# Optimization experiments

Measured on AMD Instinct MI355X. Metric: run time of the kernel, lower is better.

The kernel has to match this reference:

```python
import jax, jax.numpy as jnp
import numpy as np

BN_EPS = 1e-5


def setup_inputs() -> dict:
    key = jax.random.key(0)
    ks = jax.random.split(key, 12)
    B, N, d_e, d_a = 16, 2048, 256, 64
    s_e = 1.0 / np.sqrt(d_e)
    return {
        "x":    jax.random.normal(ks[0], (B, N, d_e), dtype=jnp.float32),
        "Wq":   jax.random.uniform(ks[1], (d_e, d_a), jnp.float32, -s_e, s_e),
        "bq":   jax.random.uniform(ks[2], (d_a,), jnp.float32, -s_e, s_e),
        "Wk":   jax.random.uniform(ks[3], (d_e, d_a), jnp.float32, -s_e, s_e),
        "bk":   jax.random.uniform(ks[4], (d_a,), jnp.float32, -s_e, s_e),
        "Wv":   jax.random.uniform(ks[5], (d_e, d_e), jnp.float32, -s_e, s_e),
        "bv":   jax.random.uniform(ks[6], (d_e,), jnp.float32, -s_e, s_e),
        "Wl":   jax.random.uniform(ks[7], (d_e, d_e), jnp.float32, -s_e, s_e),
        "bl":   jax.random.uniform(ks[8], (d_e,), jnp.float32, -s_e, s_e),
        "gamma": jnp.ones((d_e,), jnp.float32),
        "beta":  jnp.zeros((d_e,), jnp.float32),
    }


def reference(x, Wq, bq, Wk, bk, Wv, bv, Wl, bl, gamma, beta):
    # x: [B, N, d_e]
    q = x @ Wq + bq          # [B, N, d_a]
    k = x @ Wk + bk          # [B, N, d_a]
    v = x @ Wv + bv          # [B, N, d_e]
    d_a = q.shape[-1]
    # NOTE: PCT scales by d_a, not sqrt(d_a) -- faithful to the source.
    score = jnp.einsum('bnd,bmd->bnm', q, k) / jnp.asarray(d_a, q.dtype)
    score = jax.nn.softmax(score, axis=2)          # [B, N, N]
    attn = jnp.einsum('bnm,bmd->bnd', score, v)    # [B, N, d_e]
    # LBR: linear + BatchNorm1d (training-mode batch stats over B,N) + ReLU
    h = attn @ Wl + bl                             # [B, N, d_e]
    mean = jnp.mean(h, axis=(0, 1))
    var = jnp.mean((h - mean) ** 2, axis=(0, 1))   # biased variance (torch BN)
    y = jax.nn.relu((h - mean) * jax.lax.rsqrt(var + BN_EPS) * gamma + beta)
    return y + x
```

## Files before the change

### kernel.cpp

```cpp
#include <hip/hip_runtime.h>
#include <hip/hip_bf16.h>

#define B_  16
#define N_  2048
#define DE  256
#define DA  64
#define T_  (B_*N_)

typedef __attribute__((ext_vector_type(4)))  float f32x4;
typedef __attribute__((ext_vector_type(8)))  short bf16x8;
typedef unsigned short u16;
typedef unsigned long long u64;

__device__ __forceinline__ float bf2f(u16 x){
  unsigned v = ((unsigned)x) << 16;
  return __builtin_bit_cast(float, v);
}
__device__ __forceinline__ u16 f2bf(float f){
  unsigned u = __builtin_bit_cast(unsigned, f);
  u += 0x7fffu + ((u >> 16) & 1u);
  return (u16)(u >> 16);
}
__device__ __forceinline__ unsigned cvtpk(float a, float b){
  unsigned r;
  asm("v_cvt_pk_bf16_f32 %0, %1, %2" : "=v"(r) : "v"(a), "v"(b));
  return r;
}
__device__ __forceinline__ f32x4 mfma16(bf16x8 a, bf16x8 b, f32x4 c){
  return __builtin_amdgcn_mfma_f32_16x16x32_bf16(a, b, c, 0, 0, 0);
}
__device__ __forceinline__ bool is_f32(const void* gsig){
  return *(const unsigned*)gsig == 0x3F800000u;
}
__device__ __forceinline__ float gload(const void* p, long i, bool f32m){
  return f32m ? ((const float*)p)[i] : bf2f(((const u16*)p)[i]);
}

__global__ void k_prep(const void* __restrict__ Wq, const void* __restrict__ Wk,
                       const void* __restrict__ Wv, const void* __restrict__ Wl,
                       const void* __restrict__ bq, const void* __restrict__ bk,
                       const void* __restrict__ bv, const void* __restrict__ bl,
                       const void* __restrict__ gsig,
                       u16* __restrict__ Wt, u16* __restrict__ Wlt,
                       float* __restrict__ bqkv, float* __restrict__ blf){
  bool f32m = is_f32(gsig);
  int i = blockIdx.x*256 + threadIdx.x;
  if (i < 384*256){
    int n = i/256, kk = i%256;
    float v;
    if (n < 64)       v = gload(Wq, (long)kk*64 + n, f32m);
    else if (n < 128) v = gload(Wk, (long)kk*64 + (n-64), f32m);
    else              v = gload(Wv, (long)kk*256 + (n-128), f32m);
    Wt[i] = f2bf(v);
  }
  int j = i - 384*256;
  if (j >= 0 && j < 256*256){
    int n = j/256, kk = j%256;
    Wlt[j] = f2bf(gload(Wl, (long)kk*256 + n, f32m));
  }
  int m = i - (384*256 + 256*256);
  if (m >= 0 && m < 384){
    float v;
    if (m < 64)       v = gload(bq, m, f32m);
    else if (m < 128) v = gload(bk, m-64, f32m);
    else              v = gload(bv, m-128, f32m);
    bqkv[m] = v;
  }
  int p = i - (384*256 + 256*256 + 384);
  if (p >= 0 && p < 256) blf[p] = gload(bl, p, f32m);
}

__global__ __launch_bounds__(256) void k_qkv(
    const void* __restrict__ xg, const void* __restrict__ gsig,
    const u16* __restrict__ Wt, const float* __restrict__ bqkv,
    u16* __restrict__ qo, u16* __restrict__ ko, u16* __restrict__ vtt){
  __shared__ __align__(16) u16 sm[256*72];
  bool f32m = is_f32(gsig);
  int tid = threadIdx.x, lane = tid & 63, w = tid >> 6;
  int lm = lane & 15, lq = lane >> 4;
  long t0 = (long)blockIdx.x * 64;

  #pragma unroll
  for(int it=0; it<8; it++){
    int c = tid + 256*it;
    int tok = c >> 5, kk = (c & 31)*8;
    bf16x8 d;
    if (f32m){
      const float* xf = (const float*)xg + (t0+tok)*DE + kk;
      f32x4 a = *(const f32x4*)xf;
      f32x4 b2 = *(const f32x4*)(xf+4);
      #pragma unroll
      for(int j2=0;j2<4;j2++){ d[j2]=(short)f2bf(a[j2]); d[4+j2]=(short)f2bf(b2[j2]); }
    } else {
      d = *(const bf16x8*)((const u16*)xg + (t0+tok)*DE + kk);
    }
    *(bf16x8*)(sm + tok*264 + kk) = d;
  }
  __syncthreads();

  f32x4 acc[4][6];
  #pragma unroll
  for(int mt=0;mt<4;mt++)
    #pragma unroll
    for(int nt=0;nt<6;nt++){ acc[mt][nt][0]=0.f;acc[mt][nt][1]=0.f;acc[mt][nt][2]=0.f;acc[mt][nt][3]=0.f; }

  for(int s=0;s<8;s++){
    int kk = s*32 + lq*8;
    bf16x8 afr[4];
    #pragma unroll
    for(int mt=0;mt<4;mt++)
      afr[mt] = *(const bf16x8*)(sm + (mt*16+lm)*264 + kk);
    #pragma unroll
    for(int nt=0;nt<6;nt++){
      int col = w*96 + nt*16 + lm;
      bf16x8 bfr = *(const bf16x8*)(Wt + (long)col*DE + kk);
      #pragma unroll
      for(int mt=0;mt<4;mt++)
        acc[mt][nt] = mfma16(afr[mt], bfr, acc[mt][nt]);
    }
  }
  __syncthreads();

  #pragma unroll
  for(int nt=0;nt<6;nt++){
    int col = w*96 + nt*16 + lm;
    float bias = bqkv[col];
    #pragma unroll
    for(int mt=0;mt<4;mt++){
      #pragma unroll
      for(int r=0;r<4;r++){
        int tokin = mt*16 + lq*4 + r;
        u16 o = f2bf(acc[mt][nt][r] + bias);
        if (col < 64)        qo[(t0+tokin)*DA + col]      = o;
        else if (col < 128)  ko[(t0+tokin)*DA + (col-64)] = o;
        else                 sm[(col-128)*72 + tokin]     = o;
      }
    }
  }
  __syncthreads();
  int b = (int)(t0 >> 11), kt = (int)((t0 & 2047) >> 6);
  u16* tile = vtt + (long)(b*32 + kt)*16384;
  #pragma unroll
  for(int g=0; g<8; g++){
    bf16x8 d = *(const bf16x8*)(sm + tid*72 + g*8);
    *(bf16x8*)(tile + tid*64 + g*8) = d;
  }
}

__global__ __launch_bounds__(256, 2) void k_attn(
    const u16* __restrict__ qg, const u16* __restrict__ kg,
    const u16* __restrict__ vtt, u16* __restrict__ attng){
  __shared__ __align__(16) u16 P[4][64*72];
  __shared__ float lred[4][64];

  int bid = blockIdx.x;
  int b  = 2*(bid & 7) + ((bid >> 3) >> 5);
  int qb = (bid >> 3) & 31;
  int tid = threadIdx.x, lane = tid & 63, w = tid >> 6;
  int lm = lane & 15, lq = lane >> 4;

  long kb0 = (long)b * N_;
  long rb  = kb0 + qb*64;

  const float cexp = 0.0225421850f;

  const u16* qbase = qg + rb*DA;
  bf16x8 qf[4][2];
  #pragma unroll
  for(int qt=0;qt<4;qt++)
    #pragma unroll
    for(int c=0;c<2;c++)
      qf[qt][c] = *(const bf16x8*)(qbase + (long)(qt*16+lm)*DA + c*32 + lq*8);

  f32x4 o[4][4];
  #pragma unroll
  for(int rt=0;rt<4;rt++)
    #pragma unroll
    for(int nt=0;nt<4;nt++){ o[rt][nt][0]=0.f;o[rt][nt][1]=0.f;o[rt][nt][2]=0.f;o[rt][nt][3]=0.f; }
  float ls[4] = {0.f, 0.f, 0.f, 0.f};

  const u16* kptr = kg  + (kb0 + 16*w + lm)*DA + lq*8;
  const u16* vptr = vtt + (long)b*524288 + (64*w + lm)*64 + lq*8;

  #define LDS_BARRIER asm volatile("s_waitcnt lgkmcnt(0)\n\ts_barrier" ::: "memory")

  #define PHASE_A(t, K0, K1) {                                               \
    u16* Pw = P[(t)&3];                                                      \
    _Pragma("unroll")                                                        \
    for(int qt=0;qt<4;qt++){                                                 \
      f32x4 a4; a4[0]=0.f;a4[1]=0.f;a4[2]=0.f;a4[3]=0.f;                     \
      a4 = mfma16(K0, qf[qt][0], a4);                                        \
      a4 = mfma16(K1, qf[qt][1], a4);                                        \
      float e0 = exp2f(a4[0]*cexp), e1 = exp2f(a4[1]*cexp);                  \
      float e2 = exp2f(a4[2]*cexp), e3 = exp2f(a4[3]*cexp);                  \
      ls[qt] += (e0+e1)+(e2+e3);                                             \
      u64 pk = (u64)cvtpk(e0,e1) | ((u64)cvtpk(e2,e3) << 32);                \
      *(u64*)(Pw + (qt*16+lm)*72 + 16*w + 4*lq) = pk;                        \
    } }

  #define PHASE_B(t) {                                                       \
    const u16* Pr = P[(t)&3];                                                \
    const u16* vn = vptr + (long)(t)*16384;                                  \
    bf16x8 pf0[4], pf1[4];                                                   \
    _Pragma("unroll")                                                        \
    for(int rt=0;rt<4;rt++){                                                 \
      pf0[rt] = *(const bf16x8*)(Pr + (rt*16+lm)*72 + lq*8);                 \
      pf1[rt] = *(const bf16x8*)(Pr + (rt*16+lm)*72 + 32 + lq*8);            \
    }                                                                        \
    _Pragma("unroll")                                                        \
    for(int nt=0;nt<4;nt++){                                                 \
      bf16x8 v0 = *(const bf16x8*)(vn + nt*1024);                            \
      bf16x8 v1 = *(const bf16x8*)(vn + nt*1024 + 32);                       \
      _Pragma("unroll")                                                      \
      for(int rt=0;rt<4;rt++){                                               \
        o[rt][nt] = mfma16(pf0[rt], v0, o[rt][nt]);                          \
        o[rt][nt] = mfma16(pf1[rt], v1, o[rt][nt]);                          \
      }                                                                      \
    } }

  bf16x8 ka0, ka1, kb0_, kb1_;
  ka0  = *(const bf16x8*)(kptr);
  ka1  = *(const bf16x8*)(kptr + 32);
  kb0_ = *(const bf16x8*)(kptr + (long)64*DA);
  kb1_ = *(const bf16x8*)(kptr + (long)64*DA + 32);
  PHASE_A(0, ka0, ka1);
  PHASE_A(1, kb0_, kb1_);
  ka0  = *(const bf16x8*)(kptr + (long)2*64*DA);
  ka1  = *(const bf16x8*)(kptr + (long)2*64*DA + 32);
  kb0_ = *(const bf16x8*)(kptr + (long)3*64*DA);
  kb1_ = *(const bf16x8*)(kptr + (long)3*64*DA + 32);
  LDS_BARRIER;

  for(int R=1; R<16; R++){
    PHASE_B(2*R-2);
    PHASE_A(2*R,   ka0, ka1);
    PHASE_B(2*R-1);
    PHASE_A(2*R+1, kb0_, kb1_);
    int t2 = (2*R+2 < 32) ? 2*R+2 : 31;
    int t3 = (2*R+3 < 32) ? 2*R+3 : 31;
    ka0  = *(const bf16x8*)(kptr + (long)t2*64*DA);
    ka1  = *(const bf16x8*)(kptr + (long)t2*64*DA + 32);
    kb0_ = *(const bf16x8*)(kptr + (long)t3*64*DA);
    kb1_ = *(const bf16x8*)(kptr + (long)t3*64*DA + 32);
    LDS_BARRIER;
  }

  PHASE_B(30);
  PHASE_B(31);

  #undef PHASE_A
  #undef PHASE_B
  #undef LDS_BARRIER

  #pragma unroll
  for(int qt=0;qt<4;qt++){
    float s = ls[qt];
    s += __shfl_xor(s, 16, 64);
    s += __shfl_xor(s, 32, 64);
    ls[qt] = s;
  }
  if (lane < 16){
    #pragma unroll
    for(int qt=0;qt<4;qt++)
      lred[w][qt*16 + lane] = ls[qt];
  }
  __syncthreads();
  u16* abase = attng + rb*DE + 64*w;
  #pragma unroll
  for(int rt=0;rt<4;rt++){
    #pragma unroll
    for(int r=0;r<4;r++){
      int row = rt*16 + lq*4 + r;
      float inv = 1.0f / (lred[0][row] + lred[1][row] + lred[2][row] + lred[3][row]);
      #pragma unroll
      for(int nt=0;nt<4;nt++)
        abase[(long)row*DE + nt*16 + lm] = f2bf(o[rt][nt][r] * inv);
    }
  }
}

__global__ __launch_bounds__(256) void k_hgemm(
    const u16* __restrict__ attng, const u16* __restrict__ Wlt,
    const float* __restrict__ blf, u16* __restrict__ hg, float* __restrict__ stats){
  __shared__ __align__(16) u16 xs[64*264];
  int tid = threadIdx.x, lane = tid & 63, w = tid >> 6;
  int lm = lane & 15, lq = lane >> 4;
  long t0 = (long)blockIdx.x * 64;

  const u16* src = attng + t0*DE;
  #pragma unroll
  for(int i=0;i<8;i++){
    int c16 = tid + 256*i;
    int tok = c16 >> 5, kk = (c16 & 31)*8;
    *(bf16x8*)(xs + tok*264 + kk) = *(const bf16x8*)(src + (long)tok*DE + kk);
  }
  __syncthreads();

  f32x4 acc[4][4];
  #pragma unroll
  for(int mt=0;mt<4;mt++)
    #pragma unroll
    for(int nt=0;nt<4;nt++){ acc[mt][nt][0]=0.f;acc[mt][nt][1]=0.f;acc[mt][nt][2]=0.f;acc[mt][nt][3]=0.f; }

  for(int s=0;s<8;s++){
    int kk = s*32 + lq*8;
    bf16x8 afr[4];
    #pragma unroll
    for(int mt=0;mt<4;mt++)
      afr[mt] = *(const bf16x8*)(xs + (mt*16+lm)*264 + kk);
    #pragma unroll
    for(int nt=0;nt<4;nt++){
      int col = w*64 + nt*16 + lm;
      bf16x8 bfr = *(const bf16x8*)(Wlt + (long)col*DE + kk);
      #pragma unroll
      for(int mt=0;mt<4;mt++)
        acc[mt][nt] = mfma16(afr[mt], bfr, acc[mt][nt]);
    }
  }
  #pragma unroll
  for(int nt=0;nt<4;nt++){
    int col = w*64 + nt*16 + lm;
    float bias = blf[col];
    float s1 = 0.f, s2 = 0.f;
    #pragma unroll
    for(int mt=0;mt<4;mt++){
      #pragma unroll
      for(int r=0;r<4;r++){
        long tok = t0 + mt*16 + lq*4 + r;
        float val = acc[mt][nt][r] + bias;
        hg[tok*DE + col] = f2bf(val);
        s1 += val; s2 += val*val;
      }
    }
    s1 += __shfl_xor(s1, 16, 64); s2 += __shfl_xor(s2, 16, 64);
    s1 += __shfl_xor(s1, 32, 64); s2 += __shfl_xor(s2, 32, 64);
    if (lq == 0){
      atomicAdd(&stats[col], s1);
      atomicAdd(&stats[256 + col], s2);
    }
  }
}

__global__ __launch_bounds__(256) void k_apply(
    const u16* __restrict__ hg, const void* __restrict__ xg,
    const void* __restrict__ gamma, const void* __restrict__ beta,
    const float* __restrict__ stats, void* __restrict__ outg){
  __shared__ float sc[256], sh[256];
  bool f32m = is_f32(gamma);
  int tid = threadIdx.x;
  {
    const float inv_n = 1.0f/32768.0f;
    float mean = stats[tid]*inv_n;
    float var  = stats[256+tid]*inv_n - mean*mean;
    float s = gload(gamma, tid, f32m) * rsqrtf(var + 1e-5f);
    sc[tid] = s;
    sh[tid] = gload(beta, tid, f32m) - mean*s;
  }
  __syncthreads();

  long i = (long)blockIdx.x*256 + tid;
  long base = i*8;
  int ch0 = (int)(base & 255);
  bf16x8 hv = *(const bf16x8*)(hg + base);
  float xv[8];
  if (f32m){
    f32x4 a = *((const f32x4*)xg + i*2);
    f32x4 b2 = *((const f32x4*)xg + i*2 + 1);
    #pragma unroll
    for(int j=0;j<4;j++){ xv[j]=a[j]; xv[4+j]=b2[j]; }
  } else {
    bf16x8 xb = *((const bf16x8*)xg + i);
    #pragma unroll
    for(int j=0;j<8;j++) xv[j] = bf2f((u16)xb[j]);
  }
  float y[8];
  #pragma unroll
  for(int j=0;j<8;j++){
    float h = bf2f((u16)hv[j]);
    y[j] = fmaxf(h*sc[ch0+j] + sh[ch0+j], 0.f) + xv[j];
  }
  if (f32m){
    f32x4 o0, o1;
    #pragma unroll
    for(int j=0;j<4;j++){ o0[j]=y[j]; o1[j]=y[4+j]; }
    __builtin_nontemporal_store(o0, (f32x4*)outg + i*2);
    __builtin_nontemporal_store(o1, (f32x4*)outg + i*2 + 1);
  } else {
    bf16x8 ov;
    #pragma unroll
    for(int j=0;j<8;j++) ov[j] = (short)f2bf(y[j]);
    __builtin_nontemporal_store(ov, (bf16x8*)outg + i);
  }
}

extern "C" void kernel_launch(void* const* d_in, const int* in_sizes, int n_in,
                              void* d_out, int out_size, void* d_ws, size_t ws_size,
                              hipStream_t stream){
  const void* x     = d_in[0];
  const void* Wq    = d_in[1];
  const void* bq    = d_in[2];
  const void* Wk    = d_in[3];
  const void* bk    = d_in[4];
  const void* Wv    = d_in[5];
  const void* bv    = d_in[6];
  const void* Wl    = d_in[7];
  const void* bl    = d_in[8];
  const void* gamma = d_in[9];
  const void* beta  = d_in[10];

  char* ws = (char*)d_ws;
  u16*   Wt    = (u16*)  (ws + 0x0);
  u16*   Wlt   = (u16*)  (ws + 0x30000);
  float* bqkv  = (float*)(ws + 0x50000);
  float* blf   = (float*)(ws + 0x50600);
  float* stats = (float*)(ws + 0x50A00);
  u16*   qw    = (u16*)  (ws + 0x60000);
  u16*   kw    = (u16*)  (ws + 0x460000);
  u16*   vtt   = (u16*)  (ws + 0x860000);
  u16*   attnw = (u16*)  (ws + 0x1860000);
  u16*   hw    = (u16*)  (ws + 0x2860000);

  hipMemsetAsync(stats, 0, 512*sizeof(float), stream);
  k_prep  <<<643, 256, 0, stream>>>(Wq, Wk, Wv, Wl, bq, bk, bv, bl, gamma, Wt, Wlt, bqkv, blf);
  k_qkv   <<<512, 256, 0, stream>>>(x, gamma, Wt, bqkv, qw, kw, vtt);
  k_attn  <<<512, 256, 0, stream>>>(qw, kw, vtt, attnw);
  k_hgemm <<<512, 256, 0, stream>>>(attnw, Wlt, blf, hw, stats);
  k_apply <<<4096, 256, 0, stream>>>(hw, x, gamma, beta, stats, d_out);
}
```

Measured before the change: 249.8 us.

## Keep attention probabilities in registers, dropping LDS staging and barriers

The attention kernel is restructured so each wave owns 16 query rows across all 256 output columns. It permutes the K row order so the QK^T MFMA output lands directly in the A-operand layout of the PV MFMA. This removes the shared-memory P buffers, the block barriers and the cross-wave row-sum reduction. In exchange, each wave now loads the full K and V tiles itself with no software prefetch. That raises per-wave global and L2 traffic and exposes load latency, and it holds 16 accumulator tiles per wave.

```diff
diff --git a/kernel.cpp b/kernel.cpp
--- a/kernel.cpp
+++ b/kernel.cpp
@@ -9,6 +9,7 @@
 
 typedef __attribute__((ext_vector_type(4)))  float f32x4;
 typedef __attribute__((ext_vector_type(8)))  short bf16x8;
+typedef __attribute__((ext_vector_type(4)))  unsigned u32x4;
 typedef unsigned short u16;
 typedef unsigned long long u64;
 
@@ -150,9 +151,6 @@
 __global__ __launch_bounds__(256, 2) void k_attn(
     const u16* __restrict__ qg, const u16* __restrict__ kg,
     const u16* __restrict__ vtt, u16* __restrict__ attng){
-  __shared__ __align__(16) u16 P[4][64*72];
-  __shared__ float lred[4][64];
-
   int bid = blockIdx.x;
   int b  = 2*(bid & 7) + ((bid >> 3) >> 5);
   int qb = (bid >> 3) & 31;
@@ -164,118 +162,66 @@
 
   const float cexp = 0.0225421850f;
 
-  const u16* qbase = qg + rb*DA;
-  bf16x8 qf[4][2];
-  #pragma unroll
-  for(int qt=0;qt<4;qt++)
-    #pragma unroll
-    for(int c=0;c<2;c++)
-      qf[qt][c] = *(const bf16x8*)(qbase + (long)(qt*16+lm)*DA + c*32 + lq*8);
-
-  f32x4 o[4][4];
-  #pragma unroll
-  for(int rt=0;rt<4;rt++)
-    #pragma unroll
-    for(int nt=0;nt<4;nt++){ o[rt][nt][0]=0.f;o[rt][nt][1]=0.f;o[rt][nt][2]=0.f;o[rt][nt][3]=0.f; }
-  float ls[4] = {0.f, 0.f, 0.f, 0.f};
-
-  const u16* kptr = kg  + (kb0 + 16*w + lm)*DA + lq*8;
-  const u16* vptr = vtt + (long)b*524288 + (64*w + lm)*64 + lq*8;
-
-  #define LDS_BARRIER asm volatile("s_waitcnt lgkmcnt(0)\n\ts_barrier" ::: "memory")
-
-  #define PHASE_A(t, K0, K1) {                                               \
-    u16* Pw = P[(t)&3];                                                      \
-    _Pragma("unroll")                                                        \
-    for(int qt=0;qt<4;qt++){                                                 \
-      f32x4 a4; a4[0]=0.f;a4[1]=0.f;a4[2]=0.f;a4[3]=0.f;                     \
-      a4 = mfma16(K0, qf[qt][0], a4);                                        \
-      a4 = mfma16(K1, qf[qt][1], a4);                                        \
-      float e0 = exp2f(a4[0]*cexp), e1 = exp2f(a4[1]*cexp);                  \
-      float e2 = exp2f(a4[2]*cexp), e3 = exp2f(a4[3]*cexp);                  \
-      ls[qt] += (e0+e1)+(e2+e3);                                             \
-      u64 pk = (u64)cvtpk(e0,e1) | ((u64)cvtpk(e2,e3) << 32);                \
-      *(u64*)(Pw + (qt*16+lm)*72 + 16*w + 4*lq) = pk;                        \
-    } }
-
-  #define PHASE_B(t) {                                                       \
-    const u16* Pr = P[(t)&3];                                                \
-    const u16* vn = vptr + (long)(t)*16384;                                  \
-    bf16x8 pf0[4], pf1[4];                                                   \
-    _Pragma("unroll")                                                        \
-    for(int rt=0;rt<4;rt++){                                                 \
-      pf0[rt] = *(const bf16x8*)(Pr + (rt*16+lm)*72 + lq*8);                 \
-      pf1[rt] = *(const bf16x8*)(Pr + (rt*16+lm)*72 + 32 + lq*8);            \
-    }                                                                        \
-    _Pragma("unroll")                                                        \
-    for(int nt=0;nt<4;nt++){                                                 \
-      bf16x8 v0 = *(const bf16x8*)(vn + nt*1024);                            \
-      bf16x8 v1 = *(const bf16x8*)(vn + nt*1024 + 32);                       \
-      _Pragma("unroll")                                                      \
-      for(int rt=0;rt<4;rt++){                                               \
-        o[rt][nt] = mfma16(pf0[rt], v0, o[rt][nt]);                          \
-        o[rt][nt] = mfma16(pf1[rt], v1, o[rt][nt]);                          \
-      }                                                                      \
-    } }
-
-  bf16x8 ka0, ka1, kb0_, kb1_;
-  ka0  = *(const bf16x8*)(kptr);
-  ka1  = *(const bf16x8*)(kptr + 32);
-  kb0_ = *(const bf16x8*)(kptr + (long)64*DA);
-  kb1_ = *(const bf16x8*)(kptr + (long)64*DA + 32);
-  PHASE_A(0, ka0, ka1);
-  PHASE_A(1, kb0_, kb1_);
-  ka0  = *(const bf16x8*)(kptr + (long)2*64*DA);
-  ka1  = *(const bf16x8*)(kptr + (long)2*64*DA + 32);
-  kb0_ = *(const bf16x8*)(kptr + (long)3*64*DA);
-  kb1_ = *(const bf16x8*)(kptr + (long)3*64*DA + 32);
-  LDS_BARRIER;
-
-  for(int R=1; R<16; R++){
-    PHASE_B(2*R-2);
-    PHASE_A(2*R,   ka0, ka1);
-    PHASE_B(2*R-1);
-    PHASE_A(2*R+1, kb0_, kb1_);
-    int t2 = (2*R+2 < 32) ? 2*R+2 : 31;
-    int t3 = (2*R+3 < 32) ? 2*R+3 : 31;
-    ka0  = *(const bf16x8*)(kptr + (long)t2*64*DA);
-    ka1  = *(const bf16x8*)(kptr + (long)t2*64*DA + 32);
-    kb0_ = *(const bf16x8*)(kptr + (long)t3*64*DA);
-    kb1_ = *(const bf16x8*)(kptr + (long)t3*64*DA + 32);
-    LDS_BARRIER;
-  }
-
-  PHASE_B(30);
-  PHASE_B(31);
-
-  #undef PHASE_A
-  #undef PHASE_B
-  #undef LDS_BARRIER
-
-  #pragma unroll
-  for(int qt=0;qt<4;qt++){
-    float s = ls[qt];
-    s += __shfl_xor(s, 16, 64);
-    s += __shfl_xor(s, 32, 64);
-    ls[qt] = s;
-  }
-  if (lane < 16){
-    #pragma unroll
-    for(int qt=0;qt<4;qt++)
-      lred[w][qt*16 + lane] = ls[qt];
-  }
-  __syncthreads();
-  u16* abase = attng + rb*DE + 64*w;
-  #pragma unroll
-  for(int rt=0;rt<4;rt++){
-    #pragma unroll
-    for(int r=0;r<4;r++){
-      int row = rt*16 + lq*4 + r;
-      float inv = 1.0f / (lred[0][row] + lred[1][row] + lred[2][row] + lred[3][row]);
-      #pragma unroll
-      for(int nt=0;nt<4;nt++)
-        abase[(long)row*DE + nt*16 + lm] = f2bf(o[rt][nt][r] * inv);
-    }
+  const u16* qrow = qg + (rb + w*16 + lm)*DA;
+  bf16x8 qf0 = *(const bf16x8*)(qrow + lq*8);
+  bf16x8 qf1 = *(const bf16x8*)(qrow + 32 + lq*8);
+
+  f32x4 o[16];
+  #pragma unroll
+  for(int nt=0;nt<16;nt++){ o[nt][0]=0.f;o[nt][1]=0.f;o[nt][2]=0.f;o[nt][3]=0.f; }
+  float ls = 0.f;
+
+  int krA = 8*(lm>>2) + (lm&3);
+  const u16* kbase = kg + kb0*DA;
+  const u16* vbase = vtt + (long)b*524288;
+  int voff = lm*64 + lq*8;
+
+  for(int t=0; t<N_/64; t++){
+    const u16* kt_ = kbase + (long)t*64*DA;
+    const u16* vt_ = vbase + (long)t*16384 + voff;
+    #pragma unroll
+    for(int c=0;c<2;c++){
+      const u16* kr0 = kt_ + (long)(c*32 + krA)*DA + lq*8;
+      bf16x8 kA0 = *(const bf16x8*)(kr0);
+      bf16x8 kA1 = *(const bf16x8*)(kr0 + 32);
+      bf16x8 kB0 = *(const bf16x8*)(kr0 + 4*DA);
+      bf16x8 kB1 = *(const bf16x8*)(kr0 + 4*DA + 32);
+      f32x4 sA; sA[0]=0.f;sA[1]=0.f;sA[2]=0.f;sA[3]=0.f;
+      sA = mfma16(kA0, qf0, sA);
+      sA = mfma16(kA1, qf1, sA);
+      f32x4 sB; sB[0]=0.f;sB[1]=0.f;sB[2]=0.f;sB[3]=0.f;
+      sB = mfma16(kB0, qf0, sB);
+      sB = mfma16(kB1, qf1, sB);
+      float e0 = exp2f(sA[0]*cexp), e1 = exp2f(sA[1]*cexp);
+      float e2 = exp2f(sA[2]*cexp), e3 = exp2f(sA[3]*cexp);
+      float f0 = exp2f(sB[0]*cexp), f1 = exp2f(sB[1]*cexp);
+      float f2 = exp2f(sB[2]*cexp), f3 = exp2f(sB[3]*cexp);
+      ls += ((e0+e1)+(e2+e3)) + ((f0+f1)+(f2+f3));
+      u32x4 pd;
+      pd[0] = cvtpk(e0, e1);
+      pd[1] = cvtpk(e2, e3);
+      pd[2] = cvtpk(f0, f1);
+      pd[3] = cvtpk(f2, f3);
+      bf16x8 pa = __builtin_bit_cast(bf16x8, pd);
+      const u16* vc = vt_ + c*32;
+      #pragma unroll
+      for(int nt=0;nt<16;nt++)
+        o[nt] = mfma16(pa, *(const bf16x8*)(vc + nt*1024), o[nt]);
+    }
+  }
+
+  float lsr = ls;
+  lsr += __shfl_xor(lsr, 16, 64);
+  lsr += __shfl_xor(lsr, 32, 64);
+
+  u16* abase = attng + (rb + w*16)*DE;
+  #pragma unroll
+  for(int r=0;r<4;r++){
+    float inv = 1.0f / __shfl(lsr, 4*lq + r, 64);
+    int row = 4*lq + r;
+    #pragma unroll
+    for(int nt=0;nt<16;nt++)
+      abase[(long)row*DE + nt*16 + lm] = f2bf(o[nt][r] * inv);
   }
 }
 
```

Result: slower. 470.4 us (+88.3%).
